# Optimization experiments

Hardware: AMD Instinct MI355X
Metric: run time of the kernel (lower is better)

Reference implementation:

```python
import jax, jax.numpy as jnp
import numpy as np
from jax import lax

B, T, N, CIN, CH, COUT, K, KS, E = 2, 16, 2048, 32, 64, 64, 3, 3, 32768


def setup_inputs() -> dict:
    key = jax.random.key(0)
    ks = jax.random.split(key, 20)
    s = 0.05
    p = lambda k, shp: s * jax.random.normal(k, shp, dtype=jnp.float32)
    return {
        "X": jax.random.normal(ks[0], (B, T, N, CIN), dtype=jnp.float32),
        "edge_index": jax.random.randint(ks[1], (2, E), 0, N),
        "edge_weight": jax.random.uniform(ks[2], (E,), dtype=jnp.float32),
        "tc1_w1": p(ks[3], (CH, CIN, 1, KS)), "tc1_b1": p(ks[4], (CH,)),
        "tc1_w2": p(ks[5], (CH, CIN, 1, KS)), "tc1_b2": p(ks[6], (CH,)),
        "tc1_w3": p(ks[7], (CH, CIN, 1, KS)), "tc1_b3": p(ks[8], (CH,)),
        "cheb_w": p(ks[9], (K, CH, CH)), "cheb_b": p(ks[10], (CH,)),
        "tc2_w1": p(ks[11], (COUT, CH, 1, KS)), "tc2_b1": p(ks[12], (COUT,)),
        "tc2_w2": p(ks[13], (COUT, CH, 1, KS)), "tc2_b2": p(ks[14], (COUT,)),
        "tc2_w3": p(ks[15], (COUT, CH, 1, KS)), "tc2_b3": p(ks[16], (COUT,)),
        "bn_gamma": jnp.ones((N,), jnp.float32),
        "bn_beta": jnp.zeros((N,), jnp.float32),
    }


def _tconv(X, w1, b1, w2, b2, w3, b3):
    # X: (B, T, N, C) -> (B, C, N, T), gated temporal conv over last axis
    x = jnp.transpose(X, (0, 3, 2, 1))
    dn = ("NCHW", "OIHW", "NCHW")
    c = lambda w, b: lax.conv_general_dilated(x, w, (1, 1), "VALID", dimension_numbers=dn) + b[None, :, None, None]
    out = jax.nn.relu(c(w1, b1) + jax.nn.sigmoid(c(w2, b2)) + c(w3, b3))
    return jnp.transpose(out, (0, 3, 2, 1))


def _cheb(x, edge_index, edge_weight, W, b):
    # ChebConv, sym normalization, lambda_max=2 -> L_hat = -D^{-1/2} A D^{-1/2}
    row, col = edge_index[0], edge_index[1]
    w = jnp.where(row == col, 0.0, edge_weight)  # get_laplacian removes self-loops
    deg = jax.ops.segment_sum(w, row, num_segments=N)
    safe = jnp.where(deg > 0, deg, 1.0)
    dis = jnp.where(deg > 0, lax.rsqrt(safe), 0.0)
    norm = -dis[row] * w * dis[col]  # (E,)

    def prop(z):  # z: (B, T, N, C)
        zm = jnp.moveaxis(z, 2, 0)                      # (N, B, T, C)
        msg = zm[col] * norm[:, None, None, None]       # (E, B, T, C)
        agg = jax.ops.segment_sum(msg, row, num_segments=N)
        return jnp.moveaxis(agg, 0, 2)

    Tx0 = x
    out = jnp.einsum("btnc,co->btno", Tx0, W[0])
    Tx1 = prop(Tx0)
    out = out + jnp.einsum("btnc,co->btno", Tx1, W[1])
    for k in range(2, K):
        Tx2 = 2.0 * prop(Tx1) - Tx0
        out = out + jnp.einsum("btnc,co->btno", Tx2, W[k])
        Tx0, Tx1 = Tx1, Tx2
    return out + b


def reference(X, edge_index, edge_weight, tc1_w1, tc1_b1, tc1_w2, tc1_b2, tc1_w3, tc1_b3,
              cheb_w, cheb_b, tc2_w1, tc2_b1, tc2_w2, tc2_b2, tc2_w3, tc2_b3,
              bn_gamma, bn_beta):
    t1 = _tconv(X, tc1_w1, tc1_b1, tc1_w2, tc1_b2, tc1_w3, tc1_b3)   # (B, T-2, N, CH)
    t2 = jax.nn.relu(_cheb(t1, edge_index, edge_weight, cheb_w, cheb_b))
    t3 = _tconv(t2, tc2_w1, tc2_b1, tc2_w2, tc2_b2, tc2_w3, tc2_b3)  # (B, T-4, N, COUT)
    t = jnp.transpose(t3, (0, 2, 1, 3))  # (B, N, T', COUT): N is BN channel axis
    mu = jnp.mean(t, axis=(0, 2, 3), keepdims=True)
    var = jnp.var(t, axis=(0, 2, 3), keepdims=True)
    t = (t - mu) * lax.rsqrt(var + 1e-5) * bn_gamma[None, :, None, None] + bn_beta[None, :, None, None]
    return jnp.transpose(t, (0, 2, 1, 3))
```

## Files before the change

kernel.cpp:

```cpp
#include <hip/hip_runtime.h>
#include <cstdint>
#include <cstddef>

typedef unsigned short ushort_t;
typedef short bf16x8 __attribute__((ext_vector_type(8)));
typedef float f32x4 __attribute__((ext_vector_type(4)));

#define N_NODES 2048
#define E_EDGES 32768

constexpr int OFS_X     = 0;
constexpr int OFS_EW    = 2097152;
constexpr int OFS_SMALL = 2129920;
constexpr int SMALL_TOTAL = 72128;
constexpr int OFS_T1W1 = 2129920;
constexpr int OFS_T1B1 = 2136064;
constexpr int OFS_T1W2 = 2136128;
constexpr int OFS_T1B2 = 2142272;
constexpr int OFS_T1W3 = 2142336;
constexpr int OFS_T1B3 = 2148480;
constexpr int OFS_CHW  = 2148544;
constexpr int OFS_CHB  = 2160832;
constexpr int OFS_T2W1 = 2160896;
constexpr int OFS_T2B1 = 2173184;
constexpr int OFS_T2W2 = 2173248;
constexpr int OFS_T2B2 = 2185536;
constexpr int OFS_T2W3 = 2185600;
constexpr int OFS_T2B3 = 2197888;
constexpr int OFS_GAM  = 2197952;
constexpr int OFS_BET  = 2200000;
constexpr int CAN_TOTAL = 2202048;

__device__ __align__(16) ushort_t g_t1b [3670016];
__device__ __align__(16) ushort_t g_tx1b[3670016];
__device__ __align__(16) ushort_t g_tx2b[3670016];
__device__ __align__(16) ushort_t g_t2b [3670016];
__device__ __align__(16) float    g_t3 [3145728];
__device__ float    g_deg[N_NODES];
__device__ int      g_cnt[N_NODES];
__device__ int      g_cur[N_NODES];
__device__ __align__(8) int2 g_csrp[E_EDGES];
__device__ int      g_rowstart[N_NODES + 1];
__device__ __align__(16) ushort_t g_can[CAN_TOTAL];
__device__ __align__(16) ushort_t g_wb1[18432];
__device__ __align__(16) ushort_t g_wb2[36864];
__device__ __align__(16) ushort_t g_wbc[12288];

__device__ __forceinline__ float bfu(ushort_t u) { return __uint_as_float(((unsigned)u) << 16); }
__device__ __forceinline__ float lo16(unsigned u) { return __uint_as_float(u << 16); }
__device__ __forceinline__ float hi16(unsigned u) { return __uint_as_float(u & 0xffff0000u); }
__device__ __forceinline__ ushort_t f2bf(float f) {
    unsigned u = __float_as_uint(f);
    u = u + 0x7fffu + ((u >> 16) & 1u);
    return (ushort_t)(u >> 16);
}
__device__ __forceinline__ float ldin(const void* p, int i, bool isbf) {
    return isbf ? bfu(((const ushort_t*)p)[i]) : ((const float*)p)[i];
}
#define BF16_ONES_PAIR 0x3F803F80u

__global__ void convert_big_kernel(const void* __restrict__ X, const void* __restrict__ ew,
                                   const unsigned* __restrict__ gam) {
    int idx = blockIdx.x * 256 + threadIdx.x;
    bool isbf = (gam[0] == BF16_ONES_PAIR);
    if (idx < N_NODES) { g_deg[idx] = 0.f; g_cnt[idx] = 0; g_cur[idx] = 0; }
    if (idx < 2097152) {
        if (!isbf) g_can[idx] = f2bf(((const float*)X)[idx]);
    } else {
        int i = idx - 2097152;
        g_can[idx] = isbf ? ((const ushort_t*)ew)[i] : f2bf(((const float*)ew)[i]);
    }
}

struct SmallPtrs { const void* p[16]; };

__global__ void setup_a_kernel(const int* __restrict__ ei, SmallPtrs sp,
                               const unsigned* __restrict__ gam) {
    int blk = blockIdx.x;
    if (blk < 128) {
        int e = blk * 256 + threadIdx.x;
        int r = ei[e];
        int c = ei[E_EDGES + e];
        float w = (r == c) ? 0.f : bfu(g_can[OFS_EW + e]);
        atomicAdd(&g_deg[r], w);
        atomicAdd(&g_cnt[r], 1);
    } else {
        const int sizes[16] = {6144, 64, 6144, 64, 6144, 64, 12288, 64,
                               12288, 64, 12288, 64, 12288, 64, 2048, 2048};
        int idx = (blk - 128) * 256 + threadIdx.x;
        if (idx >= SMALL_TOTAL) return;
        bool isbf = (gam[0] == BF16_ONES_PAIR);
        int j = 0, local = idx;
        while (local >= sizes[j]) { local -= sizes[j]; ++j; }
        g_can[OFS_SMALL + idx] = isbf ? ((const ushort_t*)sp.p[j])[local]
                                      : f2bf(((const float*)sp.p[j])[local]);
    }
}

__global__ void scan_kernel() {
    __shared__ int part[256];
    __shared__ int pre[256];
    int t = threadIdx.x;
    int base = t * 8;
    int s = 0;
#pragma unroll
    for (int i = 0; i < 8; ++i) s += g_cnt[base + i];
    part[t] = s;
    __syncthreads();
    if (t == 0) {
        int a = 0;
        for (int i = 0; i < 256; ++i) { pre[i] = a; a += part[i]; }
    }
    __syncthreads();
    int a = pre[t];
#pragma unroll
    for (int i = 0; i < 8; ++i) { g_rowstart[base + i] = a; a += g_cnt[base + i]; }
    if (t == 255) g_rowstart[N_NODES] = a;
}

__global__ void setup_b_kernel(const int* __restrict__ ei) {
    int blk = blockIdx.x;
    if (blk < 128) {
        int e = blk * 256 + threadIdx.x;
        int r = ei[e];
        int c = ei[E_EDGES + e];
        float w = (r == c) ? 0.f : bfu(g_can[OFS_EW + e]);
        float dr = g_deg[r], dc = g_deg[c];
        float nr = dr > 0.f ? rsqrtf(dr) : 0.f;
        float nc = dc > 0.f ? rsqrtf(dc) : 0.f;
        int pos = atomicAdd(&g_cur[r], 1);
        g_csrp[g_rowstart[r] + pos] = make_int2(c, __float_as_int(-nr * w * nc));
        return;
    }
    int idx = (blk - 128) * 256 + threadIdx.x;
    if (idx < 18432) {
        int j = idx & 7, lane = (idx >> 3) & 63, kk = (idx >> 9) % 3;
        int nt = (idx / 1536) & 3, set = idx / 6144;
        int o = nt * 16 + (lane & 15);
        int k = kk * 32 + (lane >> 4) * 8 + j;
        int ci = k & 31, ks = k >> 5;
        int base = (set == 0) ? OFS_T1W1 : (set == 1) ? OFS_T1W2 : OFS_T1W3;
        g_wb1[idx] = g_can[base + o * 96 + ci * 3 + ks];
    } else if (idx < 18432 + 36864) {
        int t = idx - 18432;
        int j = t & 7, lane = (t >> 3) & 63, kk = (t >> 9) % 6;
        int nt = (t / 3072) & 3, set = t / 12288;
        int o = nt * 16 + (lane & 15);
        int k = kk * 32 + (lane >> 4) * 8 + j;
        int ci = k & 63, ks = k >> 6;
        int base = (set == 0) ? OFS_T2W1 : (set == 1) ? OFS_T2W2 : OFS_T2W3;
        g_wb2[t] = g_can[base + o * 192 + ci * 3 + ks];
    } else {
        int t = idx - 18432 - 36864;
        int j = t & 7, lane = (t >> 3) & 63, kk = (t >> 9) % 6;
        int nt = t / 3072;
        int o = nt * 16 + (lane & 15);
        int k = kk * 32 + (lane >> 4) * 8 + j;
        int sec = k >> 6, c = k & 63;
        g_wbc[t] = g_can[OFS_CHW + sec * 4096 + c * 64 + o];
    }
}

template <int LAYER>
__global__ __launch_bounds__(256) void tconv_mfma_kernel(const void* __restrict__ Xraw,
                                                         const unsigned* __restrict__ gam) {
    constexpr int CIN_  = (LAYER == 1) ? 32 : 64;
    constexpr int T_in  = (LAYER == 1) ? 16 : 14;
    constexpr int T_out = (LAYER == 1) ? 14 : 12;
    constexpr int KST   = (CIN_ * 3) / 32;
    constexpr int PADK  = (LAYER == 1) ? 104 : 200;
    constexpr int OB1 = (LAYER == 1) ? OFS_T1B1 : OFS_T2B1;
    constexpr int OB2 = (LAYER == 1) ? OFS_T1B2 : OFS_T2B2;
    constexpr int OB3 = (LAYER == 1) ? OFS_T1B3 : OFS_T2B3;

    __shared__ ushort_t xs[64 * PADK];

    const int tid = threadIdx.x;
    const int lane = tid & 63;
    const int wv = tid >> 6;
    const int m0 = blockIdx.x * 64;
    const int n0 = m0 & (N_NODES - 1);
    const int s  = m0 >> 11;
    const int b  = s / T_out;
    const int t  = s - b * T_out;

#pragma unroll
    for (int ks = 0; ks < 3; ++ks) {
        if constexpr (LAYER == 1) {
            bool isbf = (gam[0] == BF16_ONES_PAIR);
            const ushort_t* xsrc = isbf ? (const ushort_t*)Xraw : (g_can + OFS_X);
            const ushort4* src = (const ushort4*)(xsrc +
                ((size_t)(b * T_in + t + ks) * N_NODES + n0) * 32);
            for (int i = tid; i < 512; i += 256) {
                ushort4 v = src[i];
                int row = i >> 3, c4 = i & 7;
                *(ushort4*)&xs[row * PADK + ks * 32 + c4 * 4] = v;
            }
        } else {
            const ushort4* src = (const ushort4*)(g_t2b +
                ((size_t)(b * T_in + t + ks) * N_NODES + n0) * 64);
            for (int i = tid; i < 1024; i += 256) {
                ushort4 v = src[i];
                int row = i >> 4, c4 = i & 15;
                *(ushort4*)&xs[row * PADK + ks * 64 + c4 * 4] = v;
            }
        }
    }
    __syncthreads();

    const ushort_t* WB = (LAYER == 1) ? g_wb1 : g_wb2;
    f32x4 acc[3][4];
#pragma unroll
    for (int st = 0; st < 3; ++st)
#pragma unroll
        for (int nt = 0; nt < 4; ++nt) acc[st][nt] = (f32x4){0.f, 0.f, 0.f, 0.f};

    const int arow = wv * 16 + (lane & 15);
    const int kofs = (lane >> 4) * 8;
#pragma unroll
    for (int kk = 0; kk < KST; ++kk) {
        bf16x8 av = *(const bf16x8*)&xs[arow * PADK + kk * 32 + kofs];
#pragma unroll
        for (int st = 0; st < 3; ++st)
#pragma unroll
            for (int nt = 0; nt < 4; ++nt) {
                bf16x8 bv = ((const bf16x8*)WB)[((st * 4 + nt) * KST + kk) * 64 + lane];
                acc[st][nt] = __builtin_amdgcn_mfma_f32_16x16x32_bf16(av, bv, acc[st][nt], 0, 0, 0);
            }
    }

    const int col = lane & 15;
    const int quad = lane >> 4;
#pragma unroll
    for (int nt = 0; nt < 4; ++nt) {
        int o = nt * 16 + col;
        float b1 = bfu(g_can[OB1 + o]);
        float b2 = bfu(g_can[OB2 + o]);
        float b3 = bfu(g_can[OB3 + o]);
#pragma unroll
        for (int reg = 0; reg < 4; ++reg) {
            int m = m0 + wv * 16 + quad * 4 + reg;
            float q = acc[1][nt][reg] + b2;
            float v = (acc[0][nt][reg] + b1) + 1.f / (1.f + expf(-q)) + (acc[2][nt][reg] + b3);
            v = v > 0.f ? v : 0.f;
            if constexpr (LAYER == 1) g_t1b[(size_t)m * 64 + o] = f2bf(v);
            else                      g_t3 [(size_t)m * 64 + o] = v;
        }
    }
}

template <int MODE>
__global__ __launch_bounds__(256) void prop_kernel() {
    const ushort_t* __restrict__ src = (MODE == 0) ? g_t1b : g_tx1b;
    ushort_t* __restrict__ dst = (MODE == 0) ? g_tx1b : g_tx2b;
    const int n = blockIdx.x;
    const int c = threadIdx.x & 63;
    const int sg = threadIdx.x >> 6;
    const int beg = g_rowstart[n], end = g_rowstart[n + 1];
    const int s0 = sg * 7;

    float acc[7];
#pragma unroll
    for (int j = 0; j < 7; ++j) acc[j] = 0.f;

    int e = beg;
    for (; e + 2 <= end; e += 2) {
        int2 p0 = g_csrp[e];
        int2 p1 = g_csrp[e + 1];
        float w0 = __int_as_float(p0.y);
        float w1 = __int_as_float(p1.y);
        size_t b0 = ((size_t)p0.x << 6) + c;
        size_t b1 = ((size_t)p1.x << 6) + c;
#pragma unroll
        for (int j = 0; j < 7; ++j) {
            size_t so = (size_t)(s0 + j) * (N_NODES * 64);
            float v0 = bfu(src[so + b0]);
            float v1 = bfu(src[so + b1]);
            acc[j] = fmaf(w1, v1, fmaf(w0, v0, acc[j]));
        }
    }
    if (e < end) {
        int2 p0 = g_csrp[e];
        float w0 = __int_as_float(p0.y);
        size_t b0 = ((size_t)p0.x << 6) + c;
#pragma unroll
        for (int j = 0; j < 7; ++j)
            acc[j] = fmaf(w0, bfu(src[(size_t)(s0 + j) * (N_NODES * 64) + b0]), acc[j]);
    }

#pragma unroll
    for (int j = 0; j < 7; ++j) {
        size_t off = ((size_t)(s0 + j) * N_NODES + n) * 64 + c;
        if constexpr (MODE == 0) dst[off] = f2bf(acc[j]);
        else                     dst[off] = f2bf(2.f * acc[j] - bfu(g_t1b[off]));
    }
}

__global__ __launch_bounds__(256) void cheb_mfma_kernel() {
    constexpr int PADK = 200;
    __shared__ ushort_t xs[64 * PADK];

    const int tid = threadIdx.x;
    const int lane = tid & 63;
    const int wv = tid >> 6;
    const int m0 = blockIdx.x * 64;

#pragma unroll
    for (int sec = 0; sec < 3; ++sec) {
        const ushort_t* sp = (sec == 0) ? g_t1b : (sec == 1) ? g_tx1b : g_tx2b;
        const ushort4* src = (const ushort4*)(sp + (size_t)m0 * 64);
        for (int i = tid; i < 1024; i += 256) {
            ushort4 v = src[i];
            int row = i >> 4, c4 = i & 15;
            *(ushort4*)&xs[row * PADK + sec * 64 + c4 * 4] = v;
        }
    }
    __syncthreads();

    f32x4 acc[4];
#pragma unroll
    for (int nt = 0; nt < 4; ++nt) acc[nt] = (f32x4){0.f, 0.f, 0.f, 0.f};

    const int arow = wv * 16 + (lane & 15);
    const int kofs = (lane >> 4) * 8;
#pragma unroll
    for (int kk = 0; kk < 6; ++kk) {
        bf16x8 av = *(const bf16x8*)&xs[arow * PADK + kk * 32 + kofs];
#pragma unroll
        for (int nt = 0; nt < 4; ++nt) {
            bf16x8 bv = ((const bf16x8*)g_wbc)[(nt * 6 + kk) * 64 + lane];
            acc[nt] = __builtin_amdgcn_mfma_f32_16x16x32_bf16(av, bv, acc[nt], 0, 0, 0);
        }
    }

    const int col = lane & 15;
    const int quad = lane >> 4;
#pragma unroll
    for (int nt = 0; nt < 4; ++nt) {
        int o = nt * 16 + col;
        float bias = bfu(g_can[OFS_CHB + o]);
#pragma unroll
        for (int reg = 0; reg < 4; ++reg) {
            int m = m0 + wv * 16 + quad * 4 + reg;
            float v = acc[nt][reg] + bias;
            g_t2b[(size_t)m * 64 + o] = f2bf(v > 0.f ? v : 0.f);
        }
    }
}

__global__ __launch_bounds__(256) void bn_fused_kernel(void* __restrict__ outp,
                                                       const unsigned* __restrict__ gam) {
    int n = blockIdx.x;
    int tid = threadIdx.x;
    int c = tid & 63;
    int sg = tid >> 6;
    float vals[6];
    float s1 = 0.f, s2 = 0.f;
    int k = 0;
    for (int s = sg; s < 24; s += 4, ++k) {
        float v = g_t3[((size_t)(s * N_NODES + n)) * 64 + c];
        vals[k] = v;
        s1 += v;
        s2 += v * v;
    }
    __shared__ float r1[256], r2[256];
    __shared__ float sc_s, sh_s;
    r1[tid] = s1;
    r2[tid] = s2;
    __syncthreads();
    for (int st = 128; st > 0; st >>= 1) {
        if (tid < st) { r1[tid] += r1[tid + st]; r2[tid] += r2[tid + st]; }
        __syncthreads();
    }
    if (tid == 0) {
        const float inv = 1.f / 1536.f;
        float mean = r1[0] * inv;
        float var  = r2[0] * inv - mean * mean;
        float rstd = rsqrtf(var + 1e-5f);
        float g = bfu(g_can[OFS_GAM + n]), be = bfu(g_can[OFS_BET + n]);
        sc_s = rstd * g;
        sh_s = be - mean * rstd * g;
    }
    __syncthreads();
    float sc = sc_s, sh = sh_s;
    bool isbf = (gam[0] == BF16_ONES_PAIR);
    k = 0;
    for (int s = sg; s < 24; s += 4, ++k) {
        size_t off = ((size_t)(s * N_NODES + n)) * 64 + c;
        float r = vals[k] * sc + sh;
        if (isbf) ((ushort_t*)outp)[off] = f2bf(r);
        else      ((float*)outp)[off] = r;
    }
}

extern "C" void kernel_launch(void* const* d_in, const int* in_sizes, int n_in,
                              void* d_out, int out_size, void* d_ws, size_t ws_size,
                              hipStream_t stream) {
    const void* X = d_in[0];
    const int* ei = (const int*)d_in[1];
    const unsigned* gam = (const unsigned*)d_in[17];

    SmallPtrs sp;
    for (int i = 0; i < 16; ++i) sp.p[i] = d_in[3 + i];

    convert_big_kernel<<<8320, 256, 0, stream>>>(X, d_in[2], gam);
    setup_a_kernel<<<410, 256, 0, stream>>>(ei, sp, gam);
    scan_kernel<<<1, 256, 0, stream>>>();
    setup_b_kernel<<<392, 256, 0, stream>>>(ei);

    tconv_mfma_kernel<1><<<896, 256, 0, stream>>>(X, gam);

    prop_kernel<0><<<N_NODES, 256, 0, stream>>>();
    prop_kernel<1><<<N_NODES, 256, 0, stream>>>();
    cheb_mfma_kernel<<<896, 256, 0, stream>>>();

    tconv_mfma_kernel<2><<<768, 256, 0, stream>>>(X, gam);

    bn_fused_kernel<<<N_NODES, 256, 0, stream>>>(d_out, gam);
}
```

Measured before the change: 191.6 us.

## Fuse setup kernels and convert X to bf16 inside first temporal conv

Removes the full-size X/edge-weight conversion kernel by converting float X to bf16 while loading tiles in the first temporal conv, and reading edge weights directly. Degree, count and prefix scan are merged into one block that accumulates in shared memory, replacing global atomics and the separate scan launch. This cuts kernel launches and a 2M-element round trip through global memory. The trade-off is that degree accumulation now runs serially on a single block over all 32768 edges, which may be slow, although it runs alongside the small-parameter conversion blocks.

```diff
diff --git a/kernel.cpp b/kernel.cpp
--- a/kernel.cpp
+++ b/kernel.cpp
@@ -9,27 +9,24 @@
 #define N_NODES 2048
 #define E_EDGES 32768
 
-constexpr int OFS_X     = 0;
-constexpr int OFS_EW    = 2097152;
-constexpr int OFS_SMALL = 2129920;
 constexpr int SMALL_TOTAL = 72128;
-constexpr int OFS_T1W1 = 2129920;
-constexpr int OFS_T1B1 = 2136064;
-constexpr int OFS_T1W2 = 2136128;
-constexpr int OFS_T1B2 = 2142272;
-constexpr int OFS_T1W3 = 2142336;
-constexpr int OFS_T1B3 = 2148480;
-constexpr int OFS_CHW  = 2148544;
-constexpr int OFS_CHB  = 2160832;
-constexpr int OFS_T2W1 = 2160896;
-constexpr int OFS_T2B1 = 2173184;
-constexpr int OFS_T2W2 = 2173248;
-constexpr int OFS_T2B2 = 2185536;
-constexpr int OFS_T2W3 = 2185600;
-constexpr int OFS_T2B3 = 2197888;
-constexpr int OFS_GAM  = 2197952;
-constexpr int OFS_BET  = 2200000;
-constexpr int CAN_TOTAL = 2202048;
+constexpr int OFS_SMALL = 0;
+constexpr int OFS_T1W1 = 0;
+constexpr int OFS_T1B1 = 6144;
+constexpr int OFS_T1W2 = 6208;
+constexpr int OFS_T1B2 = 12352;
+constexpr int OFS_T1W3 = 12416;
+constexpr int OFS_T1B3 = 18560;
+constexpr int OFS_CHW  = 18624;
+constexpr int OFS_CHB  = 30912;
+constexpr int OFS_T2W1 = 30976;
+constexpr int OFS_T2B1 = 43264;
+constexpr int OFS_T2W2 = 43328;
+constexpr int OFS_T2B2 = 55616;
+constexpr int OFS_T2W3 = 55680;
+constexpr int OFS_T2B3 = 67968;
+constexpr int OFS_GAM  = 68032;
+constexpr int OFS_BET  = 70080;
 
 __device__ __align__(16) ushort_t g_t1b [3670016];
 __device__ __align__(16) ushort_t g_tx1b[3670016];
@@ -37,11 +34,10 @@
 __device__ __align__(16) ushort_t g_t2b [3670016];
 __device__ __align__(16) float    g_t3 [3145728];
 __device__ float    g_deg[N_NODES];
-__device__ int      g_cnt[N_NODES];
 __device__ int      g_cur[N_NODES];
 __device__ __align__(8) int2 g_csrp[E_EDGES];
 __device__ int      g_rowstart[N_NODES + 1];
-__device__ __align__(16) ushort_t g_can[CAN_TOTAL];
+__device__ __align__(16) ushort_t g_can[SMALL_TOTAL];
 __device__ __align__(16) ushort_t g_wb1[18432];
 __device__ __align__(16) ushort_t g_wb2[36864];
 __device__ __align__(16) ushort_t g_wbc[12288];
@@ -59,72 +55,64 @@
 }
 #define BF16_ONES_PAIR 0x3F803F80u
 
-__global__ void convert_big_kernel(const void* __restrict__ X, const void* __restrict__ ew,
-                                   const unsigned* __restrict__ gam) {
-    int idx = blockIdx.x * 256 + threadIdx.x;
-    bool isbf = (gam[0] == BF16_ONES_PAIR);
-    if (idx < N_NODES) { g_deg[idx] = 0.f; g_cnt[idx] = 0; g_cur[idx] = 0; }
-    if (idx < 2097152) {
-        if (!isbf) g_can[idx] = f2bf(((const float*)X)[idx]);
-    } else {
-        int i = idx - 2097152;
-        g_can[idx] = isbf ? ((const ushort_t*)ew)[i] : f2bf(((const float*)ew)[i]);
-    }
-}
-
 struct SmallPtrs { const void* p[16]; };
 
-__global__ void setup_a_kernel(const int* __restrict__ ei, SmallPtrs sp,
-                               const unsigned* __restrict__ gam) {
-    int blk = blockIdx.x;
-    if (blk < 128) {
-        int e = blk * 256 + threadIdx.x;
-        int r = ei[e];
-        int c = ei[E_EDGES + e];
-        float w = (r == c) ? 0.f : bfu(g_can[OFS_EW + e]);
-        atomicAdd(&g_deg[r], w);
-        atomicAdd(&g_cnt[r], 1);
-    } else {
+__global__ void setup1_kernel(const int* __restrict__ ei, const void* __restrict__ ew,
+                              SmallPtrs sp, const unsigned* __restrict__ gam) {
+    __shared__ float sdeg[N_NODES];
+    __shared__ int   scnt[N_NODES];
+    __shared__ int   part[256];
+    __shared__ int   pre[256];
+    const bool isbf = (gam[0] == BF16_ONES_PAIR);
+    const int tid = threadIdx.x;
+    if (blockIdx.x < 282) {
         const int sizes[16] = {6144, 64, 6144, 64, 6144, 64, 12288, 64,
                                12288, 64, 12288, 64, 12288, 64, 2048, 2048};
-        int idx = (blk - 128) * 256 + threadIdx.x;
+        int idx = blockIdx.x * 256 + tid;
         if (idx >= SMALL_TOTAL) return;
-        bool isbf = (gam[0] == BF16_ONES_PAIR);
         int j = 0, local = idx;
         while (local >= sizes[j]) { local -= sizes[j]; ++j; }
         g_can[OFS_SMALL + idx] = isbf ? ((const ushort_t*)sp.p[j])[local]
                                       : f2bf(((const float*)sp.p[j])[local]);
-    }
-}
-
-__global__ void scan_kernel() {
-    __shared__ int part[256];
-    __shared__ int pre[256];
-    int t = threadIdx.x;
-    int base = t * 8;
+        return;
+    }
+    for (int i = tid; i < N_NODES; i += 256) { sdeg[i] = 0.f; scnt[i] = 0; g_cur[i] = 0; }
+    __syncthreads();
+    for (int e = tid; e < E_EDGES; e += 256) {
+        int r = ei[e];
+        int c = ei[E_EDGES + e];
+        float w = (r == c) ? 0.f : ldin(ew, e, isbf);
+        atomicAdd(&sdeg[r], w);
+        atomicAdd(&scnt[r], 1);
+    }
+    __syncthreads();
+    int base = tid * 8;
     int s = 0;
 #pragma unroll
-    for (int i = 0; i < 8; ++i) s += g_cnt[base + i];
-    part[t] = s;
-    __syncthreads();
-    if (t == 0) {
+    for (int i = 0; i < 8; ++i) s += scnt[base + i];
+    part[tid] = s;
+    __syncthreads();
+    if (tid == 0) {
         int a = 0;
         for (int i = 0; i < 256; ++i) { pre[i] = a; a += part[i]; }
     }
     __syncthreads();
-    int a = pre[t];
-#pragma unroll
-    for (int i = 0; i < 8; ++i) { g_rowstart[base + i] = a; a += g_cnt[base + i]; }
-    if (t == 255) g_rowstart[N_NODES] = a;
-}
-
-__global__ void setup_b_kernel(const int* __restrict__ ei) {
+    int a = pre[tid];
+#pragma unroll
+    for (int i = 0; i < 8; ++i) { g_rowstart[base + i] = a; a += scnt[base + i]; }
+    if (tid == 255) g_rowstart[N_NODES] = a;
+    for (int i = tid; i < N_NODES; i += 256) g_deg[i] = sdeg[i];
+}
+
+__global__ void setup2_kernel(const int* __restrict__ ei, const void* __restrict__ ew,
+                              const unsigned* __restrict__ gam) {
     int blk = blockIdx.x;
     if (blk < 128) {
+        bool isbf = (gam[0] == BF16_ONES_PAIR);
         int e = blk * 256 + threadIdx.x;
         int r = ei[e];
         int c = ei[E_EDGES + e];
-        float w = (r == c) ? 0.f : bfu(g_can[OFS_EW + e]);
+        float w = (r == c) ? 0.f : ldin(ew, e, isbf);
         float dr = g_deg[r], dc = g_deg[c];
         float nr = dr > 0.f ? rsqrtf(dr) : 0.f;
         float nc = dc > 0.f ? rsqrtf(dc) : 0.f;
@@ -187,14 +175,24 @@
 #pragma unroll
     for (int ks = 0; ks < 3; ++ks) {
         if constexpr (LAYER == 1) {
-            bool isbf = (gam[0] == BF16_ONES_PAIR);
-            const ushort_t* xsrc = isbf ? (const ushort_t*)Xraw : (g_can + OFS_X);
-            const ushort4* src = (const ushort4*)(xsrc +
-                ((size_t)(b * T_in + t + ks) * N_NODES + n0) * 32);
-            for (int i = tid; i < 512; i += 256) {
-                ushort4 v = src[i];
-                int row = i >> 3, c4 = i & 7;
-                *(ushort4*)&xs[row * PADK + ks * 32 + c4 * 4] = v;
+            const bool isbf = (gam[0] == BF16_ONES_PAIR);
+            const size_t elo = ((size_t)(b * T_in + t + ks) * N_NODES + n0) * 32;
+            if (isbf) {
+                const ushort4* src = (const ushort4*)((const ushort_t*)Xraw + elo);
+                for (int i = tid; i < 512; i += 256) {
+                    ushort4 v = src[i];
+                    int row = i >> 3, c4 = i & 7;
+                    *(ushort4*)&xs[row * PADK + ks * 32 + c4 * 4] = v;
+                }
+            } else {
+                const float4* src = (const float4*)((const float*)Xraw + elo);
+                for (int i = tid; i < 512; i += 256) {
+                    float4 f = src[i];
+                    ushort4 v;
+                    v.x = f2bf(f.x); v.y = f2bf(f.y); v.z = f2bf(f.z); v.w = f2bf(f.w);
+                    int row = i >> 3, c4 = i & 7;
+                    *(ushort4*)&xs[row * PADK + ks * 32 + c4 * 4] = v;
+                }
             }
         } else {
             const ushort4* src = (const ushort4*)(g_t2b +
@@ -398,15 +396,14 @@
                               hipStream_t stream) {
     const void* X = d_in[0];
     const int* ei = (const int*)d_in[1];
+    const void* ew = d_in[2];
     const unsigned* gam = (const unsigned*)d_in[17];
 
     SmallPtrs sp;
     for (int i = 0; i < 16; ++i) sp.p[i] = d_in[3 + i];
 
-    convert_big_kernel<<<8320, 256, 0, stream>>>(X, d_in[2], gam);
-    setup_a_kernel<<<410, 256, 0, stream>>>(ei, sp, gam);
-    scan_kernel<<<1, 256, 0, stream>>>();
-    setup_b_kernel<<<392, 256, 0, stream>>>(ei);
+    setup1_kernel<<<283, 256, 0, stream>>>(ei, ew, sp, gam);
+    setup2_kernel<<<392, 256, 0, stream>>>(ei, ew, gam);
 
     tconv_mfma_kernel<1><<<896, 256, 0, stream>>>(X, gam);
 
```

New measurement: 245.5 us. 28.1% more time.
